# Kernel optimization log

Hardware: AMD Instinct MI355X
Metric: run time of the kernel (lower is better)

## Reference

```python
import jax, jax.numpy as jnp
from jax import lax
import numpy as np

B0 = 2          # batch
S = 32          # spatial grid side; L = S*S + 2
L = S * S + 2
DM = 256        # d_model
ED = 512        # d_inner = expand_factor * d_model
N = 16          # d_state
R = 16          # dt_rank = ceil(d_model/16)
K = 4           # d_conv


def _dwconv(x, w, b):
    # x: (B, L, ED) -> causal depthwise conv1d, kernel K, left-pad K-1 (== torch pad K-1 then [:, :, :L])
    xt = jnp.transpose(x, (0, 2, 1))  # (B, ED, L)
    o = lax.conv_general_dilated(xt, w, (1,), [(K - 1, 0)],
                                 feature_group_count=ED,
                                 dimension_numbers=('NCH', 'OIH', 'NCH'))
    return jnp.transpose(o + b[None, :, None], (0, 2, 1))


def _ssm(x, Alog, Dp, xp_w, dt_w, dt_b):
    # x: (B, L, ED); selective scan (mamba.py math, pscan=True path)
    A = -jnp.exp(Alog)                       # (ED, N)
    dBC = x @ xp_w.T                          # (B, L, R+2N)
    delta = jax.nn.softplus(dBC[..., :R] @ dt_w.T + dt_b)  # (B, L, ED)
    Bm = dBC[..., R:R + N]                    # (B, L, N)
    Cm = dBC[..., R + N:]                     # (B, L, N)
    dA = jnp.exp(delta[..., None] * A)        # (B, L, ED, N)
    dBx = (delta * x)[..., None] * Bm[:, :, None, :]  # (B, L, ED, N)

    def comb(e1, e2):
        a1, b1 = e1
        a2, b2 = e2
        return a1 * a2, a2 * b1 + b2

    _, hs = lax.associative_scan(comb, (dA, dBx), axis=1)  # h_t = dA_t*h_{t-1} + dBx_t
    return jnp.einsum('blen,bln->ble', hs, Cm) + Dp * x


def _cross(t):
    # keep first/last token, transpose the SxS interior grid (row-major <-> col-major)
    b, l, d = t.shape
    inner = t[:, 1:-1].reshape(b, S, S, d).transpose(0, 2, 1, 3).reshape(b, S * S, d)
    return jnp.concatenate([t[:, :1], inner, t[:, -1:]], axis=1)


def _branch(xz, cw, cb, xp, dw, db, Al, Dp):
    xa, za = jnp.split(xz, 2, axis=-1)
    xa = jax.nn.silu(_dwconv(xa, cw, cb))
    return _ssm(xa, Al, Dp, xp, dw, db) * jax.nn.silu(za)


def _forward(x, in_w, out_w, *p):
    xz = x @ in_w.T  # (B, L, 2*ED)
    (cwa, cba, xpa, dwa, dba, Ala, Da,
     cwb, cbb, xpb, dwb, dbb, Alb, Db,
     cwc, cbc, xpc, dwc, dbc, Alc, Dc,
     cwd, cbd, xpd, dwd, dbd, Ald, Dd) = p
    ga = _branch(xz, cwa, cba, xpa, dwa, dba, Ala, Da)                # forward scan
    gb = _branch(xz[:, ::-1], cwb, cbb, xpb, dwb, dbb, Alb, Db)       # reversed scan
    xzc = _cross(xz)
    gc = _branch(xzc, cwc, cbc, xpc, dwc, dbc, Alc, Dc)               # transposed scan
    gd = _branch(xzc[:, ::-1], cwd, cbd, xpd, dwd, dbd, Ald, Dd)      # reversed-transposed scan
    # gating commutes with token permutations, so reassemble gated outputs
    y = (ga + gb[:, ::-1] + _cross(gc) + _cross(gd)[:, ::-1]) * 0.25  # divide_output=True
    return y @ out_w.T


def setup_inputs() -> dict:
    keys = jax.random.split(jax.random.key(0), 64)
    it = iter(keys)

    def nrm(shape, scale=0.02):
        return scale * jax.random.normal(next(it), shape, dtype=jnp.float32)

    d = {}
    d['x'] = jax.random.normal(next(it), (B0, L, DM), dtype=jnp.float32)
    d['in_w'] = nrm((2 * ED, DM))
    d['out_w'] = nrm((DM, ED))
    std = R ** -0.5
    for s in ['a', 'b', 'c', 'd']:
        d[f'conv_w_{s}'] = nrm((ED, 1, K), 0.1)
        d[f'conv_b_{s}'] = jnp.zeros((ED,), jnp.float32)
        d[f'xp_w_{s}'] = nrm((R + 2 * N, ED))
        d[f'dt_w_{s}'] = jax.random.uniform(next(it), (ED, R), minval=-std, maxval=std, dtype=jnp.float32)
        dt = jnp.exp(jax.random.uniform(next(it), (ED,), dtype=jnp.float32)
                     * (np.float32(np.log(0.1)) - np.float32(np.log(0.001))) + np.float32(np.log(0.001)))
        d[f'dt_b_{s}'] = dt + jnp.log(-jnp.expm1(-dt))  # inverse-softplus init
        d[f'Alog_{s}'] = jnp.log(jnp.tile(jnp.arange(1, N + 1, dtype=jnp.float32), (ED, 1)))
        d[f'D_{s}'] = jnp.ones((ED,), jnp.float32)
    return d


def reference(x, in_w, out_w,
              conv_w_a, conv_b_a, xp_w_a, dt_w_a, dt_b_a, Alog_a, D_a,
              conv_w_b, conv_b_b, xp_w_b, dt_w_b, dt_b_b, Alog_b, D_b,
              conv_w_c, conv_b_c, xp_w_c, dt_w_c, dt_b_c, Alog_c, D_c,
              conv_w_d, conv_b_d, xp_w_d, dt_w_d, dt_b_d, Alog_d, D_d):
    return _forward(x, in_w, out_w,
                    conv_w_a, conv_b_a, xp_w_a, dt_w_a, dt_b_a, Alog_a, D_a,
                    conv_w_b, conv_b_b, xp_w_b, dt_w_b, dt_b_b, Alog_b, D_b,
                    conv_w_c, conv_b_c, xp_w_c, dt_w_c, dt_b_c, Alog_c, D_c,
                    conv_w_d, conv_b_d, xp_w_d, dt_w_d, dt_b_d, Alog_d, D_d)
```

## Files before the change

kernel.cpp:

```cpp
#include <hip/hip_runtime.h>
#include <math.h>

#define LL 1026
#define EDim 512
#define MM 2052
#define NC 16
#define LC 64

struct Params {
  const float* cw[4];
  const float* cb[4];
  const float* xpw[4];
  const float* dtw[4];
  const float* dtb[4];
  const float* Al[4];
  const float* Dp[4];
};

__device__ __forceinline__ int sigma_map(int branch, int l) {
  if (branch & 1) l = LL - 1 - l;
  if (branch & 2) {
    if (l > 0 && l < LL - 1) {
      int p = l - 1;
      l = 1 + ((p & 31) << 5) + (p >> 5);
    }
  }
  return l;
}

__device__ __forceinline__ float silu_f(float v) {
  return v * __builtin_amdgcn_rcpf(1.f + __expf(-v));
}
__device__ __forceinline__ float softplus_f(float s) {
  return fmaxf(s, 0.f) + __logf(1.f + __expf(-fabsf(s)));
}

template<int CTRL>
__device__ __forceinline__ float dpp_mov0(float x) {
  int r = __builtin_amdgcn_update_dpp(0, __float_as_int(x), CTRL, 0xF, 0xF, false);
  return __int_as_float(r);
}

__device__ __forceinline__ float red16(float r) {
  r += dpp_mov0<0xB1>(r);
  r += dpp_mov0<0x4E>(r);
  r += dpp_mov0<0x114>(r);
  r += dpp_mov0<0x118>(r);
  return r;
}

__global__ __launch_bounds__(256) void k1_gemm_in(
    const float* __restrict__ x, const float* __restrict__ w,
    float* __restrict__ xa, float* __restrict__ sz) {
  __shared__ float As[32][68];
  __shared__ float Bs[32][68];
  const int t = threadIdx.x;
  const int tx = t & 15, ty = t >> 4;
  const int m0 = blockIdx.x * 64, n0 = blockIdx.y * 64;
  float acc[4][4] = {};
  for (int k0 = 0; k0 < 256; k0 += 32) {
    #pragma unroll
    for (int p = 0; p < 2; ++p) {
      int f = t + p * 256;
      int row = f >> 3, cf = f & 7;
      int gr = m0 + row; gr = gr < MM ? gr : MM - 1;
      float4 v = *(const float4*)(x + (size_t)gr * 256 + k0 + cf * 4);
      As[cf*4+0][row] = v.x; As[cf*4+1][row] = v.y;
      As[cf*4+2][row] = v.z; As[cf*4+3][row] = v.w;
      int gn = n0 + row;
      float4 u = *(const float4*)(w + (size_t)gn * 256 + k0 + cf * 4);
      Bs[cf*4+0][row] = u.x; Bs[cf*4+1][row] = u.y;
      Bs[cf*4+2][row] = u.z; Bs[cf*4+3][row] = u.w;
    }
    __syncthreads();
    #pragma unroll
    for (int k = 0; k < 32; ++k) {
      float4 av = *(const float4*)&As[k][ty*4];
      float4 bv = *(const float4*)&Bs[k][tx*4];
      float a0 = av.x, a1 = av.y, a2 = av.z, a3 = av.w;
      float b0 = bv.x, b1 = bv.y, b2 = bv.z, b3 = bv.w;
      acc[0][0]=fmaf(a0,b0,acc[0][0]); acc[0][1]=fmaf(a0,b1,acc[0][1]); acc[0][2]=fmaf(a0,b2,acc[0][2]); acc[0][3]=fmaf(a0,b3,acc[0][3]);
      acc[1][0]=fmaf(a1,b0,acc[1][0]); acc[1][1]=fmaf(a1,b1,acc[1][1]); acc[1][2]=fmaf(a1,b2,acc[1][2]); acc[1][3]=fmaf(a1,b3,acc[1][3]);
      acc[2][0]=fmaf(a2,b0,acc[2][0]); acc[2][1]=fmaf(a2,b1,acc[2][1]); acc[2][2]=fmaf(a2,b2,acc[2][2]); acc[2][3]=fmaf(a2,b3,acc[2][3]);
      acc[3][0]=fmaf(a3,b0,acc[3][0]); acc[3][1]=fmaf(a3,b1,acc[3][1]); acc[3][2]=fmaf(a3,b2,acc[3][2]); acc[3][3]=fmaf(a3,b3,acc[3][3]);
    }
    __syncthreads();
  }
  #pragma unroll
  for (int i = 0; i < 4; ++i) {
    int gm = m0 + ty*4 + i;
    if (gm < MM) {
      #pragma unroll
      for (int j = 0; j < 4; ++j) {
        int gn = n0 + tx*4 + j;
        float v = acc[i][j];
        if (gn < 512) xa[(size_t)gm*512 + gn] = v;
        else          sz[(size_t)gm*512 + gn - 512] = silu_f(v);
      }
    }
  }
}

__global__ __launch_bounds__(256) void k2_branch(
    Params P, const float* __restrict__ xa,
    float* __restrict__ xac, float* __restrict__ delta, float* __restrict__ bcg,
    float* __restrict__ acc_out) {
  __shared__ float xcS[16][516];
  __shared__ float dBCs[16][49];
  const int t = threadIdx.x;
  const int l0 = blockIdx.x * 16;
  const int b  = blockIdx.y;
  const int br = blockIdx.z;
  const int e0 = 2 * t;

  if (br == 0) {
    float* ab = acc_out + ((size_t)b * LL + l0) * 512;
    int nmax = (LL - l0 < 16 ? LL - l0 : 16) * 512;
    for (int idx = t; idx < nmax; idx += 256) ab[idx] = 0.f;
  }

  const float* cw = P.cw[br];
  const float w00 = cw[e0*4+0], w01 = cw[e0*4+1], w02 = cw[e0*4+2], w03 = cw[e0*4+3];
  const float w10 = cw[(e0+1)*4+0], w11 = cw[(e0+1)*4+1], w12 = cw[(e0+1)*4+2], w13 = cw[(e0+1)*4+3];
  const float cb0 = P.cb[br][e0], cb1 = P.cb[br][e0+1];
  const float* xab = xa + (size_t)b * LL * 512;
  const size_t obase = (size_t)(br*2 + b) * LL;

  float h0x=0,h0y=0,h1x=0,h1y=0,h2x=0,h2y=0,h3x=0,h3y=0;
  for (int i = -3; i < 16; ++i) {
    int l = l0 + i;
    float cx = 0.f, cy = 0.f;
    if (l >= 0 && l < LL) {
      int pos = sigma_map(br, l);
      float2 v = *(const float2*)(xab + (size_t)pos * 512 + e0);
      cx = v.x; cy = v.y;
    }
    h0x=h1x; h0y=h1y; h1x=h2x; h1y=h2y; h2x=h3x; h2y=h3y; h3x=cx; h3y=cy;
    if (i >= 0) {
      float o0 = fmaf(w00,h0x, fmaf(w01,h1x, fmaf(w02,h2x, fmaf(w03,h3x, cb0))));
      float o1 = fmaf(w10,h0y, fmaf(w11,h1y, fmaf(w12,h2y, fmaf(w13,h3y, cb1))));
      o0 = silu_f(o0); o1 = silu_f(o1);
      *(float2*)&xcS[i][e0] = make_float2(o0, o1);
      if (l < LL)
        *(float2*)(xac + (obase + l) * 512 + e0) = make_float2(o0, o1);
    }
  }
  __syncthreads();

  const int rowi = t & 15;
  const int r0 = t >> 4;
  const float* xpw = P.xpw[br];
  const float4* xr4 = (const float4*)&xcS[rowi][0];
  const float4* wa = (const float4*)(xpw + (size_t)r0 * 512);
  const float4* wb = (const float4*)(xpw + (size_t)(r0 + 16) * 512);
  const float4* wc = (const float4*)(xpw + (size_t)(r0 + 32) * 512);
  float acc0 = 0.f, acc1 = 0.f, acc2 = 0.f;
  #pragma unroll 8
  for (int e4 = 0; e4 < 128; ++e4) {
    float4 xv = xr4[e4];
    float4 a = wa[e4], bb = wb[e4], c = wc[e4];
    acc0 = fmaf(xv.x,a.x, fmaf(xv.y,a.y, fmaf(xv.z,a.z, fmaf(xv.w,a.w, acc0))));
    acc1 = fmaf(xv.x,bb.x,fmaf(xv.y,bb.y,fmaf(xv.z,bb.z,fmaf(xv.w,bb.w,acc1))));
    acc2 = fmaf(xv.x,c.x, fmaf(xv.y,c.y, fmaf(xv.z,c.z, fmaf(xv.w,c.w, acc2))));
  }
  dBCs[rowi][r0]      = acc0;
  dBCs[rowi][r0 + 16] = acc1;
  dBCs[rowi][r0 + 32] = acc2;
  __syncthreads();

  for (int idx = t; idx < 512; idx += 256) {
    int row = idx >> 5, c = idx & 31;
    int l = l0 + row;
    if (l < LL) bcg[(obase + l)*32 + c] = dBCs[row][16 + c];
  }

  const float* dtw = P.dtw[br];
  float dw0[16], dw1[16];
  #pragma unroll
  for (int r = 0; r < 16; ++r) { dw0[r] = dtw[e0*16 + r]; dw1[r] = dtw[(e0+1)*16 + r]; }
  const float db0 = P.dtb[br][e0], db1 = P.dtb[br][e0+1];
  for (int row = 0; row < 16; ++row) {
    int l = l0 + row;
    if (l >= LL) break;
    float s0 = db0, s1 = db1;
    #pragma unroll
    for (int r = 0; r < 16; ++r) {
      float d = dBCs[row][r];
      s0 = fmaf(d, dw0[r], s0);
      s1 = fmaf(d, dw1[r], s1);
    }
    *(float2*)(delta + (obase + l)*512 + e0) = make_float2(softplus_f(s0), softplus_f(s1));
  }
}

__global__ __launch_bounds__(256) void k3a_chunk(
    Params P, const float* __restrict__ xac, const float* __restrict__ delta,
    const float* __restrict__ bcg, float* __restrict__ Pc, float* __restrict__ Qc) {
  __shared__ float dT[16][36], xT[16][36], bT[16][36];
  const int t = threadIdx.x;
  const int eL = t >> 4, n = t & 15;
  const int e0 = blockIdx.x * 16;
  const int b = blockIdx.y;
  const int br = blockIdx.z / NC, c = blockIdx.z % NC;
  const size_t sbase = (size_t)(br*2 + b) * LL;
  const float* dl = delta + sbase * 512;
  const float* xc = xac + sbase * 512;
  const float* bc = bcg + sbase * 32;
  const float A_en = -__expf(P.Al[br][(e0 + eL)*16 + n]);
  const int l0 = c * LC;
  const int lend = (c == NC-1) ? LL : (l0 + LC);
  float h = 0.f, dsum = 0.f;

  for (int c0 = l0; c0 < lend; c0 += 32) {
    {
      const int idx = t & 127;
      const int s = idx >> 2, q = idx & 3;
      const int l = c0 + s;
      float4 v = make_float4(0.f,0.f,0.f,0.f);
      if (t < 128) {
        if (l < lend) v = *(const float4*)(dl + (size_t)l*512 + e0 + q*4);
        dT[q*4+0][s]=v.x; dT[q*4+1][s]=v.y; dT[q*4+2][s]=v.z; dT[q*4+3][s]=v.w;
        float4 u = make_float4(0.f,0.f,0.f,0.f);
        if (l < lend) u = *(const float4*)(bc + (size_t)l*32 + q*4);
        bT[q*4+0][s]=u.x; bT[q*4+1][s]=u.y; bT[q*4+2][s]=u.z; bT[q*4+3][s]=u.w;
      } else {
        if (l < lend) v = *(const float4*)(xc + (size_t)l*512 + e0 + q*4);
        xT[q*4+0][s]=v.x; xT[q*4+1][s]=v.y; xT[q*4+2][s]=v.z; xT[q*4+3][s]=v.w;
      }
    }
    __syncthreads();
    #pragma unroll
    for (int s4 = 0; s4 < 32; s4 += 4) {
      float4 dv = *(const float4*)&dT[eL][s4];
      float4 xv = *(const float4*)&xT[eL][s4];
      float4 bv = *(const float4*)&bT[n][s4];
      float g0 = __expf(dv.x*A_en), g1 = __expf(dv.y*A_en);
      float g2 = __expf(dv.z*A_en), g3 = __expf(dv.w*A_en);
      dsum += (dv.x+dv.y)+(dv.z+dv.w);
      h = fmaf(g0, h, dv.x*xv.x*bv.x);
      h = fmaf(g1, h, dv.y*xv.y*bv.y);
      h = fmaf(g2, h, dv.z*xv.z*bv.z);
      h = fmaf(g3, h, dv.w*xv.w*bv.w);
    }
    __syncthreads();
  }
  size_t oi = ((((size_t)(br*2 + b)*NC + c)*32 + blockIdx.x)*256 + t);
  Pc[oi] = __expf(dsum * A_en);
  Qc[oi] = h;
}

__global__ __launch_bounds__(256) void k3b_scan(
    Params P, const float* __restrict__ xac, const float* __restrict__ delta,
    const float* __restrict__ bcg, const float* __restrict__ sz,
    const float* __restrict__ Pc, const float* __restrict__ Qc,
    float* __restrict__ acc_out) {
  __shared__ float dT[16][36], xT[16][36], bT[16][36], cT[16][36];
  __shared__ float yb[16][36];
  const int t = threadIdx.x;
  const int eL = t >> 4, n = t & 15;
  const int e0 = blockIdx.x * 16;
  const int b = blockIdx.y;
  const int br = blockIdx.z / NC, c = blockIdx.z % NC;
  const size_t sbase = (size_t)(br*2 + b) * LL;
  const float* dl = delta + sbase * 512;
  const float* xc = xac + sbase * 512;
  const float* bc = bcg + sbase * 32;
  const float A_en = -__expf(P.Al[br][(e0 + eL)*16 + n]);
  const float Dval = P.Dp[br][e0 + (t & 15)];
  const float* szb = sz + (size_t)b * LL * 512;
  float* ab = acc_out + (size_t)b * LL * 512;

  float h = 0.f;
  for (int cc = 0; cc < c; ++cc) {
    size_t ii = ((((size_t)(br*2 + b)*NC + cc)*32 + blockIdx.x)*256 + t);
    h = fmaf(Pc[ii], h, Qc[ii]);
  }

  const int l0c = c * LC;
  const int lend = (c == NC-1) ? LL : (l0c + LC);
  for (int c0 = l0c; c0 < lend; c0 += 32) {
    {
      const int idx = t & 127;
      const int s = idx >> 2, q = idx & 3;
      const int l = c0 + s;
      float4 v = make_float4(0.f,0.f,0.f,0.f);
      if (t < 128) {
        if (l < lend) v = *(const float4*)(dl + (size_t)l*512 + e0 + q*4);
        dT[q*4+0][s]=v.x; dT[q*4+1][s]=v.y; dT[q*4+2][s]=v.z; dT[q*4+3][s]=v.w;
      } else {
        if (l < lend) v = *(const float4*)(xc + (size_t)l*512 + e0 + q*4);
        xT[q*4+0][s]=v.x; xT[q*4+1][s]=v.y; xT[q*4+2][s]=v.z; xT[q*4+3][s]=v.w;
      }
    }
    {
      const int s = t >> 3, q = t & 7;
      const int l = c0 + s;
      float4 u = make_float4(0.f,0.f,0.f,0.f);
      if (l < lend) u = *(const float4*)(bc + (size_t)l*32 + q*4);
      if (q < 4) {
        bT[q*4+0][s]=u.x; bT[q*4+1][s]=u.y; bT[q*4+2][s]=u.z; bT[q*4+3][s]=u.w;
      } else {
        int q4 = (q-4)*4;
        cT[q4+0][s]=u.x; cT[q4+1][s]=u.y; cT[q4+2][s]=u.z; cT[q4+3][s]=u.w;
      }
    }
    __syncthreads();

    #pragma unroll
    for (int s4 = 0; s4 < 32; s4 += 4) {
      float4 dv = *(const float4*)&dT[eL][s4];
      float4 xv = *(const float4*)&xT[eL][s4];
      float4 bv = *(const float4*)&bT[n][s4];
      float4 cv = *(const float4*)&cT[n][s4];
      float r0, r1, r2, r3;
      h = fmaf(__expf(dv.x*A_en), h, dv.x*xv.x*bv.x); r0 = red16(h*cv.x);
      h = fmaf(__expf(dv.y*A_en), h, dv.y*xv.y*bv.y); r1 = red16(h*cv.y);
      h = fmaf(__expf(dv.z*A_en), h, dv.z*xv.z*bv.z); r2 = red16(h*cv.z);
      h = fmaf(__expf(dv.w*A_en), h, dv.w*xv.w*bv.w); r3 = red16(h*cv.w);
      if (n == 15) *(float4*)&yb[eL][s4] = make_float4(r0, r1, r2, r3);
    }
    __syncthreads();

    #pragma unroll
    for (int p = 0; p < 2; ++p) {
      int idx = t + p*256;
      int s = idx >> 4, ee = idx & 15;
      int l = c0 + s;
      if (l < lend) {
        float yv = fmaf(Dval, xT[ee][s], yb[ee][s]);
        int pos = sigma_map(br, l);
        float szv = szb[(size_t)pos * 512 + e0 + ee];
        atomicAdd(ab + (size_t)pos * 512 + e0 + ee, 0.25f * yv * szv);
      }
    }
    __syncthreads();
  }
}

__global__ __launch_bounds__(256) void k4_gemm_out(
    const float* __restrict__ acc_in, const float* __restrict__ w,
    float* __restrict__ out) {
  __shared__ float As[32][38];
  __shared__ float Bs[32][38];
  const int t = threadIdx.x;
  const int tx = t & 15, ty = t >> 4;
  const int m0 = blockIdx.x * 32, n0 = blockIdx.y * 32;
  float acc[2][2] = {};
  for (int k0 = 0; k0 < 512; k0 += 32) {
    #pragma unroll
    for (int p = 0; p < 4; ++p) {
      int idx = t + p*256;
      int row = idx >> 5, kk = idx & 31;
      int gm = m0 + row; gm = gm < MM ? gm : MM - 1;
      As[kk][row] = acc_in[(size_t)gm*512 + k0 + kk];
    }
    #pragma unroll
    for (int p = 0; p < 4; ++p) {
      int idx = t + p*256;
      int row = idx >> 5, kk = idx & 31;
      Bs[kk][row] = w[(size_t)(n0 + row)*512 + k0 + kk];
    }
    __syncthreads();
    #pragma unroll
    for (int k = 0; k < 32; ++k) {
      float2 av = *(const float2*)&As[k][ty*2];
      float2 bv = *(const float2*)&Bs[k][tx*2];
      acc[0][0]=fmaf(av.x,bv.x,acc[0][0]); acc[0][1]=fmaf(av.x,bv.y,acc[0][1]);
      acc[1][0]=fmaf(av.y,bv.x,acc[1][0]); acc[1][1]=fmaf(av.y,bv.y,acc[1][1]);
    }
    __syncthreads();
  }
  #pragma unroll
  for (int i = 0; i < 2; ++i) {
    int gm = m0 + ty*2 + i;
    if (gm < MM) {
      #pragma unroll
      for (int j = 0; j < 2; ++j)
        out[(size_t)gm*256 + n0 + tx*2 + j] = acc[i][j];
    }
  }
}

extern "C" void kernel_launch(void* const* d_in, const int* in_sizes, int n_in,
                              void* d_out, int out_size, void* d_ws, size_t ws_size,
                              hipStream_t stream) {
  const float* x    = (const float*)d_in[0];
  const float* in_w = (const float*)d_in[1];
  const float* out_w= (const float*)d_in[2];
  Params prm;
  for (int s = 0; s < 4; ++s) {
    prm.cw[s]  = (const float*)d_in[3 + s*7 + 0];
    prm.cb[s]  = (const float*)d_in[3 + s*7 + 1];
    prm.xpw[s] = (const float*)d_in[3 + s*7 + 2];
    prm.dtw[s] = (const float*)d_in[3 + s*7 + 3];
    prm.dtb[s] = (const float*)d_in[3 + s*7 + 4];
    prm.Al[s]  = (const float*)d_in[3 + s*7 + 5];
    prm.Dp[s]  = (const float*)d_in[3 + s*7 + 6];
  }
  float* ws = (float*)d_ws;
  const size_t SZ1 = (size_t)MM * 512;
  float* xa   = ws;
  float* szp  = ws + SZ1;
  float* xac  = ws + 2*SZ1;
  float* dlt  = ws + 6*SZ1;
  float* bc   = ws + 10*SZ1;
  float* acc  = ws + 10*SZ1 + (size_t)4*MM*32;
  float* Pc   = acc + SZ1;
  float* Qc   = Pc + (size_t)8*NC*32*256;

  k1_gemm_in<<<dim3(33, 16), 256, 0, stream>>>(x, in_w, xa, szp);
  k2_branch <<<dim3(65, 2, 4), 256, 0, stream>>>(prm, xa, xac, dlt, bc, acc);
  k3a_chunk <<<dim3(32, 2, 4*NC), 256, 0, stream>>>(prm, xac, dlt, bc, Pc, Qc);
  k3b_scan  <<<dim3(32, 2, 4*NC), 256, 0, stream>>>(prm, xac, dlt, bc, szp, Pc, Qc, acc);
  k4_gemm_out<<<dim3(65, 8), 256, 0, stream>>>(acc, out_w, (float*)d_out);
}
```

Before: 279.3 us.

## Split conv/projection kernel and shrink GEMM tiles for more blocks

The fused conv+x_proj kernel is split into a conv kernel with 8-row tiles and a projection kernel that reloads the conv output from global memory into shared memory. The input GEMM tile is narrowed to 64x32 and the output GEMM tile to 16x32, roughly doubling the grid sizes. The goal is to fill more compute units on this small problem, at the cost of an extra kernel launch, an extra global round trip for the conv output, and lower per-thread register reuse in the GEMMs.

```diff
diff --git a/kernel.cpp b/kernel.cpp
--- a/kernel.cpp
+++ b/kernel.cpp
@@ -53,11 +53,11 @@
     const float* __restrict__ x, const float* __restrict__ w,
     float* __restrict__ xa, float* __restrict__ sz) {
   __shared__ float As[32][68];
-  __shared__ float Bs[32][68];
+  __shared__ float Bs[32][36];
   const int t = threadIdx.x;
   const int tx = t & 15, ty = t >> 4;
-  const int m0 = blockIdx.x * 64, n0 = blockIdx.y * 64;
-  float acc[4][4] = {};
+  const int m0 = blockIdx.x * 64, n0 = blockIdx.y * 32;
+  float acc[4][2] = {};
   for (int k0 = 0; k0 < 256; k0 += 32) {
     #pragma unroll
     for (int p = 0; p < 2; ++p) {
@@ -67,8 +67,10 @@
       float4 v = *(const float4*)(x + (size_t)gr * 256 + k0 + cf * 4);
       As[cf*4+0][row] = v.x; As[cf*4+1][row] = v.y;
       As[cf*4+2][row] = v.z; As[cf*4+3][row] = v.w;
-      int gn = n0 + row;
-      float4 u = *(const float4*)(w + (size_t)gn * 256 + k0 + cf * 4);
+    }
+    {
+      int row = t >> 3, cf = t & 7;
+      float4 u = *(const float4*)(w + (size_t)(n0 + row) * 256 + k0 + cf * 4);
       Bs[cf*4+0][row] = u.x; Bs[cf*4+1][row] = u.y;
       Bs[cf*4+2][row] = u.z; Bs[cf*4+3][row] = u.w;
     }
@@ -76,13 +78,11 @@
     #pragma unroll
     for (int k = 0; k < 32; ++k) {
       float4 av = *(const float4*)&As[k][ty*4];
-      float4 bv = *(const float4*)&Bs[k][tx*4];
-      float a0 = av.x, a1 = av.y, a2 = av.z, a3 = av.w;
-      float b0 = bv.x, b1 = bv.y, b2 = bv.z, b3 = bv.w;
-      acc[0][0]=fmaf(a0,b0,acc[0][0]); acc[0][1]=fmaf(a0,b1,acc[0][1]); acc[0][2]=fmaf(a0,b2,acc[0][2]); acc[0][3]=fmaf(a0,b3,acc[0][3]);
-      acc[1][0]=fmaf(a1,b0,acc[1][0]); acc[1][1]=fmaf(a1,b1,acc[1][1]); acc[1][2]=fmaf(a1,b2,acc[1][2]); acc[1][3]=fmaf(a1,b3,acc[1][3]);
-      acc[2][0]=fmaf(a2,b0,acc[2][0]); acc[2][1]=fmaf(a2,b1,acc[2][1]); acc[2][2]=fmaf(a2,b2,acc[2][2]); acc[2][3]=fmaf(a2,b3,acc[2][3]);
-      acc[3][0]=fmaf(a3,b0,acc[3][0]); acc[3][1]=fmaf(a3,b1,acc[3][1]); acc[3][2]=fmaf(a3,b2,acc[3][2]); acc[3][3]=fmaf(a3,b3,acc[3][3]);
+      float2 bv = *(const float2*)&Bs[k][tx*2];
+      acc[0][0]=fmaf(av.x,bv.x,acc[0][0]); acc[0][1]=fmaf(av.x,bv.y,acc[0][1]);
+      acc[1][0]=fmaf(av.y,bv.x,acc[1][0]); acc[1][1]=fmaf(av.y,bv.y,acc[1][1]);
+      acc[2][0]=fmaf(av.z,bv.x,acc[2][0]); acc[2][1]=fmaf(av.z,bv.y,acc[2][1]);
+      acc[3][0]=fmaf(av.w,bv.x,acc[3][0]); acc[3][1]=fmaf(av.w,bv.y,acc[3][1]);
     }
     __syncthreads();
   }
@@ -91,8 +91,8 @@
     int gm = m0 + ty*4 + i;
     if (gm < MM) {
       #pragma unroll
-      for (int j = 0; j < 4; ++j) {
-        int gn = n0 + tx*4 + j;
+      for (int j = 0; j < 2; ++j) {
+        int gn = n0 + tx*2 + j;
         float v = acc[i][j];
         if (gn < 512) xa[(size_t)gm*512 + gn] = v;
         else          sz[(size_t)gm*512 + gn - 512] = silu_f(v);
@@ -101,22 +101,19 @@
   }
 }
 
-__global__ __launch_bounds__(256) void k2_branch(
-    Params P, const float* __restrict__ xa,
-    float* __restrict__ xac, float* __restrict__ delta, float* __restrict__ bcg,
+__global__ __launch_bounds__(256) void k2a_conv(
+    Params P, const float* __restrict__ xa, float* __restrict__ xac,
     float* __restrict__ acc_out) {
-  __shared__ float xcS[16][516];
-  __shared__ float dBCs[16][49];
-  const int t = threadIdx.x;
-  const int l0 = blockIdx.x * 16;
+  const int t = threadIdx.x;
+  const int l0 = blockIdx.x * 8;
   const int b  = blockIdx.y;
   const int br = blockIdx.z;
   const int e0 = 2 * t;
 
-  if (br == 0) {
+  if (br == 0 && l0 < LL) {
+    int nrow = LL - l0; if (nrow > 8) nrow = 8;
     float* ab = acc_out + ((size_t)b * LL + l0) * 512;
-    int nmax = (LL - l0 < 16 ? LL - l0 : 16) * 512;
-    for (int idx = t; idx < nmax; idx += 256) ab[idx] = 0.f;
+    for (int idx = t; idx < nrow * 512; idx += 256) ab[idx] = 0.f;
   }
 
   const float* cw = P.cw[br];
@@ -124,10 +121,11 @@
   const float w10 = cw[(e0+1)*4+0], w11 = cw[(e0+1)*4+1], w12 = cw[(e0+1)*4+2], w13 = cw[(e0+1)*4+3];
   const float cb0 = P.cb[br][e0], cb1 = P.cb[br][e0+1];
   const float* xab = xa + (size_t)b * LL * 512;
-  const size_t obase = (size_t)(br*2 + b) * LL;
+  float* xob = xac + ((size_t)(br*2 + b) * LL) * 512;
 
   float h0x=0,h0y=0,h1x=0,h1y=0,h2x=0,h2y=0,h3x=0,h3y=0;
-  for (int i = -3; i < 16; ++i) {
+  #pragma unroll
+  for (int i = -3; i < 8; ++i) {
     int l = l0 + i;
     float cx = 0.f, cy = 0.f;
     if (l >= 0 && l < LL) {
@@ -136,14 +134,34 @@
       cx = v.x; cy = v.y;
     }
     h0x=h1x; h0y=h1y; h1x=h2x; h1y=h2y; h2x=h3x; h2y=h3y; h3x=cx; h3y=cy;
-    if (i >= 0) {
+    if (i >= 0 && l < LL) {
       float o0 = fmaf(w00,h0x, fmaf(w01,h1x, fmaf(w02,h2x, fmaf(w03,h3x, cb0))));
       float o1 = fmaf(w10,h0y, fmaf(w11,h1y, fmaf(w12,h2y, fmaf(w13,h3y, cb1))));
-      o0 = silu_f(o0); o1 = silu_f(o1);
-      *(float2*)&xcS[i][e0] = make_float2(o0, o1);
-      if (l < LL)
-        *(float2*)(xac + (obase + l) * 512 + e0) = make_float2(o0, o1);
-    }
+      *(float2*)(xob + (size_t)l * 512 + e0) = make_float2(silu_f(o0), silu_f(o1));
+    }
+  }
+}
+
+__global__ __launch_bounds__(256) void k2b_proj(
+    Params P, const float* __restrict__ xac,
+    float* __restrict__ delta, float* __restrict__ bcg) {
+  __shared__ float xcS[16][516];
+  __shared__ float dBCs[16][49];
+  const int t = threadIdx.x;
+  const int l0 = blockIdx.x * 16;
+  const int b  = blockIdx.y;
+  const int br = blockIdx.z;
+  const int e0 = 2 * t;
+  const size_t obase = (size_t)(br*2 + b) * LL;
+
+  #pragma unroll
+  for (int p = 0; p < 8; ++p) {
+    int idx = t + p*256;
+    int row = idx >> 7, c4 = idx & 127;
+    int l = l0 + row;
+    float4 v = make_float4(0.f,0.f,0.f,0.f);
+    if (l < LL) v = *(const float4*)(xac + (obase + l)*512 + c4*4);
+    *(float4*)&xcS[row][c4*4] = v;
   }
   __syncthreads();
 
@@ -340,15 +358,15 @@
 __global__ __launch_bounds__(256) void k4_gemm_out(
     const float* __restrict__ acc_in, const float* __restrict__ w,
     float* __restrict__ out) {
-  __shared__ float As[32][38];
-  __shared__ float Bs[32][38];
+  __shared__ float As[32][20];
+  __shared__ float Bs[32][36];
   const int t = threadIdx.x;
   const int tx = t & 15, ty = t >> 4;
-  const int m0 = blockIdx.x * 32, n0 = blockIdx.y * 32;
-  float acc[2][2] = {};
+  const int m0 = blockIdx.x * 16, n0 = blockIdx.y * 32;
+  float a0 = 0.f, a1 = 0.f;
   for (int k0 = 0; k0 < 512; k0 += 32) {
     #pragma unroll
-    for (int p = 0; p < 4; ++p) {
+    for (int p = 0; p < 2; ++p) {
       int idx = t + p*256;
       int row = idx >> 5, kk = idx & 31;
       int gm = m0 + row; gm = gm < MM ? gm : MM - 1;
@@ -363,21 +381,17 @@
     __syncthreads();
     #pragma unroll
     for (int k = 0; k < 32; ++k) {
-      float2 av = *(const float2*)&As[k][ty*2];
+      float av = As[k][ty];
       float2 bv = *(const float2*)&Bs[k][tx*2];
-      acc[0][0]=fmaf(av.x,bv.x,acc[0][0]); acc[0][1]=fmaf(av.x,bv.y,acc[0][1]);
-      acc[1][0]=fmaf(av.y,bv.x,acc[1][0]); acc[1][1]=fmaf(av.y,bv.y,acc[1][1]);
-    }
-    __syncthreads();
-  }
-  #pragma unroll
-  for (int i = 0; i < 2; ++i) {
-    int gm = m0 + ty*2 + i;
-    if (gm < MM) {
-      #pragma unroll
-      for (int j = 0; j < 2; ++j)
-        out[(size_t)gm*256 + n0 + tx*2 + j] = acc[i][j];
-    }
+      a0 = fmaf(av, bv.x, a0);
+      a1 = fmaf(av, bv.y, a1);
+    }
+    __syncthreads();
+  }
+  int gm = m0 + ty;
+  if (gm < MM) {
+    out[(size_t)gm*256 + n0 + tx*2 + 0] = a0;
+    out[(size_t)gm*256 + n0 + tx*2 + 1] = a1;
   }
 }
 
@@ -408,9 +422,10 @@
   float* Pc   = acc + SZ1;
   float* Qc   = Pc + (size_t)8*NC*32*256;
 
-  k1_gemm_in<<<dim3(33, 16), 256, 0, stream>>>(x, in_w, xa, szp);
-  k2_branch <<<dim3(65, 2, 4), 256, 0, stream>>>(prm, xa, xac, dlt, bc, acc);
+  k1_gemm_in<<<dim3(33, 32), 256, 0, stream>>>(x, in_w, xa, szp);
+  k2a_conv  <<<dim3(129, 2, 4), 256, 0, stream>>>(prm, xa, xac, acc);
+  k2b_proj  <<<dim3(65, 2, 4), 256, 0, stream>>>(prm, xac, dlt, bc);
   k3a_chunk <<<dim3(32, 2, 4*NC), 256, 0, stream>>>(prm, xac, dlt, bc, Pc, Qc);
   k3b_scan  <<<dim3(32, 2, 4*NC), 256, 0, stream>>>(prm, xac, dlt, bc, szp, Pc, Qc, acc);
-  k4_gemm_out<<<dim3(65, 8), 256, 0, stream>>>(acc, out_w, (float*)d_out);
-}
+  k4_gemm_out<<<dim3(129, 8), 256, 0, stream>>>(acc, out_w, (float*)d_out);
+}
```

Result: slower. 298.1 us (+6.7%).

## Split conv and projection into separate kernels and add occupancy launch bounds

Applied to the files above, without the earlier changes.

The fused conv+projection kernel is split into a conv kernel over 8-row tiles with more blocks and a projection kernel that reloads the conv output from global memory into shared memory. The conv kernel's loop is unrolled. Minimum-blocks-per-CU hints are added to all kernels to steer register allocation toward higher occupancy. The split adds one kernel launch and a round trip of the conv output through global memory in exchange for more parallelism in the conv stage.

```diff
diff --git a/kernel.cpp b/kernel.cpp
--- a/kernel.cpp
+++ b/kernel.cpp
@@ -49,7 +49,7 @@
   return r;
 }
 
-__global__ __launch_bounds__(256) void k1_gemm_in(
+__global__ __launch_bounds__(256, 2) void k1_gemm_in(
     const float* __restrict__ x, const float* __restrict__ w,
     float* __restrict__ xa, float* __restrict__ sz) {
   __shared__ float As[32][68];
@@ -101,22 +101,19 @@
   }
 }
 
-__global__ __launch_bounds__(256) void k2_branch(
-    Params P, const float* __restrict__ xa,
-    float* __restrict__ xac, float* __restrict__ delta, float* __restrict__ bcg,
+__global__ __launch_bounds__(256, 4) void k2a_conv(
+    Params P, const float* __restrict__ xa, float* __restrict__ xac,
     float* __restrict__ acc_out) {
-  __shared__ float xcS[16][516];
-  __shared__ float dBCs[16][49];
-  const int t = threadIdx.x;
-  const int l0 = blockIdx.x * 16;
+  const int t = threadIdx.x;
+  const int l0 = blockIdx.x * 8;
   const int b  = blockIdx.y;
   const int br = blockIdx.z;
   const int e0 = 2 * t;
 
-  if (br == 0) {
+  if (br == 0 && l0 < LL) {
+    int nrow = LL - l0; if (nrow > 8) nrow = 8;
     float* ab = acc_out + ((size_t)b * LL + l0) * 512;
-    int nmax = (LL - l0 < 16 ? LL - l0 : 16) * 512;
-    for (int idx = t; idx < nmax; idx += 256) ab[idx] = 0.f;
+    for (int idx = t; idx < nrow * 512; idx += 256) ab[idx] = 0.f;
   }
 
   const float* cw = P.cw[br];
@@ -124,10 +121,11 @@
   const float w10 = cw[(e0+1)*4+0], w11 = cw[(e0+1)*4+1], w12 = cw[(e0+1)*4+2], w13 = cw[(e0+1)*4+3];
   const float cb0 = P.cb[br][e0], cb1 = P.cb[br][e0+1];
   const float* xab = xa + (size_t)b * LL * 512;
-  const size_t obase = (size_t)(br*2 + b) * LL;
+  float* xob = xac + ((size_t)(br*2 + b) * LL) * 512;
 
   float h0x=0,h0y=0,h1x=0,h1y=0,h2x=0,h2y=0,h3x=0,h3y=0;
-  for (int i = -3; i < 16; ++i) {
+  #pragma unroll
+  for (int i = -3; i < 8; ++i) {
     int l = l0 + i;
     float cx = 0.f, cy = 0.f;
     if (l >= 0 && l < LL) {
@@ -136,14 +134,34 @@
       cx = v.x; cy = v.y;
     }
     h0x=h1x; h0y=h1y; h1x=h2x; h1y=h2y; h2x=h3x; h2y=h3y; h3x=cx; h3y=cy;
-    if (i >= 0) {
+    if (i >= 0 && l < LL) {
       float o0 = fmaf(w00,h0x, fmaf(w01,h1x, fmaf(w02,h2x, fmaf(w03,h3x, cb0))));
       float o1 = fmaf(w10,h0y, fmaf(w11,h1y, fmaf(w12,h2y, fmaf(w13,h3y, cb1))));
-      o0 = silu_f(o0); o1 = silu_f(o1);
-      *(float2*)&xcS[i][e0] = make_float2(o0, o1);
-      if (l < LL)
-        *(float2*)(xac + (obase + l) * 512 + e0) = make_float2(o0, o1);
-    }
+      *(float2*)(xob + (size_t)l * 512 + e0) = make_float2(silu_f(o0), silu_f(o1));
+    }
+  }
+}
+
+__global__ __launch_bounds__(256, 2) void k2b_proj(
+    Params P, const float* __restrict__ xac,
+    float* __restrict__ delta, float* __restrict__ bcg) {
+  __shared__ float xcS[16][516];
+  __shared__ float dBCs[16][49];
+  const int t = threadIdx.x;
+  const int l0 = blockIdx.x * 16;
+  const int b  = blockIdx.y;
+  const int br = blockIdx.z;
+  const int e0 = 2 * t;
+  const size_t obase = (size_t)(br*2 + b) * LL;
+
+  #pragma unroll
+  for (int p = 0; p < 8; ++p) {
+    int idx = t + p*256;
+    int row = idx >> 7, c4 = idx & 127;
+    int l = l0 + row;
+    float4 v = make_float4(0.f,0.f,0.f,0.f);
+    if (l < LL) v = *(const float4*)(xac + (obase + l)*512 + c4*4);
+    *(float4*)&xcS[row][c4*4] = v;
   }
   __syncthreads();
 
@@ -193,7 +211,7 @@
   }
 }
 
-__global__ __launch_bounds__(256) void k3a_chunk(
+__global__ __launch_bounds__(256, 4) void k3a_chunk(
     Params P, const float* __restrict__ xac, const float* __restrict__ delta,
     const float* __restrict__ bcg, float* __restrict__ Pc, float* __restrict__ Qc) {
   __shared__ float dT[16][36], xT[16][36], bT[16][36];
@@ -249,7 +267,7 @@
   Qc[oi] = h;
 }
 
-__global__ __launch_bounds__(256) void k3b_scan(
+__global__ __launch_bounds__(256, 4) void k3b_scan(
     Params P, const float* __restrict__ xac, const float* __restrict__ delta,
     const float* __restrict__ bcg, const float* __restrict__ sz,
     const float* __restrict__ Pc, const float* __restrict__ Qc,
@@ -337,7 +355,7 @@
   }
 }
 
-__global__ __launch_bounds__(256) void k4_gemm_out(
+__global__ __launch_bounds__(256, 2) void k4_gemm_out(
     const float* __restrict__ acc_in, const float* __restrict__ w,
     float* __restrict__ out) {
   __shared__ float As[32][38];
@@ -409,7 +427,8 @@
   float* Qc   = Pc + (size_t)8*NC*32*256;
 
   k1_gemm_in<<<dim3(33, 16), 256, 0, stream>>>(x, in_w, xa, szp);
-  k2_branch <<<dim3(65, 2, 4), 256, 0, stream>>>(prm, xa, xac, dlt, bc, acc);
+  k2a_conv  <<<dim3(129, 2, 4), 256, 0, stream>>>(prm, xa, xac, acc);
+  k2b_proj  <<<dim3(65, 2, 4), 256, 0, stream>>>(prm, xac, dlt, bc);
   k3a_chunk <<<dim3(32, 2, 4*NC), 256, 0, stream>>>(prm, xac, dlt, bc, Pc, Qc);
   k3b_scan  <<<dim3(32, 2, 4*NC), 256, 0, stream>>>(prm, xac, dlt, bc, szp, Pc, Qc, acc);
   k4_gemm_out<<<dim3(65, 8), 256, 0, stream>>>(acc, out_w, (float*)d_out);
```

Result: no change. 281.2 us (+0.7%).
